# Performance work log

Measured on AMD Instinct MI355X. Metric: run time of the kernel, lower is better.

The kernel has to match this reference:

```python
import jax, jax.numpy as jnp
import numpy as np

N_NODES = 50000
N_EDGES = 800000
NODE_DIM = 128
EMBED_DIM = 128


def _gcn_conv(x, W, b, src, dst):
    """GCNConv: y = D^{-1/2} (A + I) D^{-1/2} X W + b (unit edge weights)."""
    n = x.shape[0]
    xw = x @ W  # [N, out]
    loop = jnp.arange(n, dtype=src.dtype)
    src2 = jnp.concatenate([src, loop])  # self-loops appended
    dst2 = jnp.concatenate([dst, loop])
    w2 = jnp.ones(src2.shape[0], dtype=xw.dtype)
    deg = jax.ops.segment_sum(w2, dst2, num_segments=n)
    dinv = jnp.where(deg > 0, jax.lax.rsqrt(deg), jnp.zeros_like(deg))
    norm = dinv[src2] * w2 * dinv[dst2]  # [E+N]
    out = jax.ops.segment_sum(norm[:, None] * xw[src2], dst2, num_segments=n)
    return out + b


def setup_inputs() -> dict:
    key = jax.random.key(0)
    ks = jax.random.split(key, 20)
    inp = {
        'node_feat': jax.random.normal(ks[0], (N_NODES, NODE_DIM), dtype=jnp.float32),
        'src': jax.random.randint(ks[1], (N_EDGES,), 0, N_NODES, dtype=jnp.int64) if jax.config.jax_enable_x64 else jax.random.randint(ks[1], (N_EDGES,), 0, N_NODES),
        'dst': jax.random.randint(ks[2], (N_EDGES,), 0, N_NODES),
        'h': jax.random.normal(ks[3], (N_NODES, EMBED_DIM), dtype=jnp.float32),
    }
    sc_in = 1.0 / np.sqrt(NODE_DIM)
    sc_2e = 1.0 / np.sqrt(2 * EMBED_DIM)
    sc_e = 1.0 / np.sqrt(EMBED_DIM)
    # conv weight/bias + gate linear weight/bias for z, r, h gates
    for i, g in enumerate(['z', 'r', 'hh']):
        inp[f'Wc_{g}'] = jax.random.normal(ks[4 + 4 * i], (NODE_DIM, EMBED_DIM), dtype=jnp.float32) * sc_in
        inp[f'bc_{g}'] = jnp.zeros((EMBED_DIM,), dtype=jnp.float32)
        inp[f'Wl_{g}'] = jax.random.normal(ks[5 + 4 * i], (2 * EMBED_DIM, EMBED_DIM), dtype=jnp.float32) * sc_2e
        inp[f'bl_{g}'] = jnp.zeros((EMBED_DIM,), dtype=jnp.float32)
    inp['W_lin'] = jax.random.normal(ks[16], (EMBED_DIM, EMBED_DIM), dtype=jnp.float32) * sc_e
    inp['b_lin'] = jnp.zeros((EMBED_DIM,), dtype=jnp.float32)
    return inp


def reference(node_feat, src, dst, h,
              Wc_z, bc_z, Wl_z, bl_z,
              Wc_r, bc_r, Wl_r, bl_r,
              Wc_hh, bc_hh, Wl_hh, bl_hh,
              W_lin, b_lin):
    # TGCN GRU cell
    cz = _gcn_conv(node_feat, Wc_z, bc_z, src, dst)
    Z = jax.nn.sigmoid(jnp.concatenate([cz, h], axis=1) @ Wl_z + bl_z)
    cr = _gcn_conv(node_feat, Wc_r, bc_r, src, dst)
    R = jax.nn.sigmoid(jnp.concatenate([cr, h], axis=1) @ Wl_r + bl_r)
    ch = _gcn_conv(node_feat, Wc_hh, bc_hh, src, dst)
    H_tilde = jnp.tanh(jnp.concatenate([ch, h * R], axis=1) @ Wl_hh + bl_hh)
    h_0 = Z * h + (1.0 - Z) * H_tilde
    # wrapper: relu + linear
    z_out = jax.nn.relu(h_0) @ W_lin + b_lin
    return (z_out, h_0)
```

## Files before the change

kernel.cpp:

```cpp
#include <hip/hip_runtime.h>
#include <math.h>

#define NN 50000
#define DD 128
#define EE 800000

typedef __attribute__((ext_vector_type(8))) short short8;
typedef __attribute__((ext_vector_type(4))) float f32x4;

__device__ __forceinline__ ushort f2bf(float f) {
    union { float f; unsigned u; } v; v.f = f;
    unsigned r = v.u + 0x7FFF + ((v.u >> 16) & 1);
    return (ushort)(r >> 16);
}

__global__ void k_cvt_deg(const float* __restrict__ X, ushort* __restrict__ Xb,
                          const int* __restrict__ dste, int* __restrict__ deg) {
    int i = blockIdx.x * 256 + threadIdx.x;
    float4 v = ((const float4*)X)[i];
    ushort4 u;
    u.x = f2bf(v.x); u.y = f2bf(v.y); u.z = f2bf(v.z); u.w = f2bf(v.w);
    ((ushort4*)Xb)[i] = u;
    if (i < EE) atomicAdd(&deg[dste[i]], 1);
}

__global__ void k_alloc(const int* __restrict__ deg, int* __restrict__ off,
                        int* __restrict__ cursor, float* __restrict__ dinv) {
    int n = blockIdx.x * 256 + threadIdx.x;
    int lane = threadIdx.x & 63;
    int d = (n < NN) ? deg[n] : 0;
    int x = d;
    #pragma unroll
    for (int o = 1; o < 64; o <<= 1) {
        int y = __shfl_up(x, o);
        if (lane >= o) x += y;
    }
    int total = __shfl(x, 63);
    int base = 0;
    if (lane == 0) base = atomicAdd(cursor, total);
    base = __shfl(base, 0);
    if (n < NN) {
        off[n] = base + x - d;
        dinv[n] = rsqrtf((float)d + 1.0f);
    }
}

__global__ void k_fill(const int* __restrict__ src, const int* __restrict__ dst,
                       const int* __restrict__ off, int* __restrict__ cur,
                       int* __restrict__ csr) {
    int e = blockIdx.x * 256 + threadIdx.x;
    if (e < EE) {
        int d = dst[e];
        int slot = atomicAdd(&cur[d], 1);
        csr[off[d] + slot] = src[e];
    }
}

__global__ __launch_bounds__(256) void k_gather(const ushort* __restrict__ Xb,
                                                const int* __restrict__ csr,
                                                const int* __restrict__ off,
                                                const int* __restrict__ deg,
                                                const float* __restrict__ dinv,
                                                ushort* __restrict__ AXb) {
    int tid = blockIdx.x * 256 + threadIdx.x;
    int n = tid >> 6, lane = tid & 63;
    if (n >= NN) return;
    float dd = dinv[n];
    uint a = *((const uint*)(Xb + (size_t)n * 128 + lane * 2));
    float acc0 = dd * dd * __uint_as_float(a << 16);
    float acc1 = dd * dd * __uint_as_float(a & 0xffff0000u);
    int o = off[n], cnt = deg[n];
    int i = 0;
    for (; i + 8 <= cnt; i += 8) {
        int s[8];
        #pragma unroll
        for (int u = 0; u < 8; u++) s[u] = csr[o + i + u];
        uint v[8];
        #pragma unroll
        for (int u = 0; u < 8; u++) v[u] = *((const uint*)(Xb + (size_t)s[u] * 128 + lane * 2));
        float c[8];
        #pragma unroll
        for (int u = 0; u < 8; u++) c[u] = dinv[s[u]] * dd;
        #pragma unroll
        for (int u = 0; u < 8; u++) {
            acc0 += c[u] * __uint_as_float(v[u] << 16);
            acc1 += c[u] * __uint_as_float(v[u] & 0xffff0000u);
        }
    }
    for (; i < cnt; i++) {
        int s = csr[o + i];
        float c = dinv[s] * dd;
        uint v = *((const uint*)(Xb + (size_t)s * 128 + lane * 2));
        acc0 += c * __uint_as_float(v << 16);
        acc1 += c * __uint_as_float(v & 0xffff0000u);
    }
    ushort2 u2; u2.x = f2bf(acc0); u2.y = f2bf(acc1);
    *((ushort2*)(AXb + (size_t)n * 128 + lane * 2)) = u2;
}

__global__ void k_prep(const float* __restrict__ Wc_z, const float* __restrict__ Wl_z,
                       const float* __restrict__ bc_z, const float* __restrict__ bl_z,
                       const float* __restrict__ Wc_r, const float* __restrict__ Wl_r,
                       const float* __restrict__ bc_r, const float* __restrict__ bl_r,
                       const float* __restrict__ Wc_h, const float* __restrict__ Wl_h,
                       const float* __restrict__ bc_h, const float* __restrict__ bl_h,
                       const float* __restrict__ W_lin,
                       ushort* __restrict__ WAs, ushort* __restrict__ WBs,
                       ushort* __restrict__ WLs, float* __restrict__ bA,
                       float* __restrict__ bB) {
    int idx = blockIdx.x * 256 + threadIdx.x;
    if (idx < 65536) {
        int k = idx >> 8, c = idx & 255, cc = c & 127;
        const float* Wc = (c < 128) ? Wc_z : Wc_r;
        const float* Wl = (c < 128) ? Wl_z : Wl_r;
        float v;
        if (k < 128) {
            float s = 0.f;
            for (int j = 0; j < 128; j++) s += Wc[k * 128 + j] * Wl[j * 128 + cc];
            v = s;
        } else {
            v = Wl[k * 128 + cc];
        }
        WAs[(k >> 5) * 8192 + (c >> 4) * 512 + (((k >> 3) & 3) * 16 + (c & 15)) * 8 + (k & 7)] = f2bf(v);
    } else if (idx < 98304) {
        int i2 = idx - 65536;
        int k = i2 >> 7, c = i2 & 127;
        float v;
        if (k < 128) {
            float s = 0.f;
            for (int j = 0; j < 128; j++) s += Wc_h[k * 128 + j] * Wl_h[j * 128 + c];
            v = s;
        } else {
            v = Wl_h[k * 128 + c];
        }
        WBs[(k >> 5) * 4096 + (c >> 4) * 512 + (((k >> 3) & 3) * 16 + (c & 15)) * 8 + (k & 7)] = f2bf(v);
    } else if (idx < 114688) {
        int i3 = idx - 98304;
        int k = i3 >> 7, c = i3 & 127;
        WLs[(k >> 5) * 4096 + (c >> 4) * 512 + (((k >> 3) & 3) * 16 + (c & 15)) * 8 + (k & 7)] = f2bf(W_lin[k * 128 + c]);
    } else if (idx < 114944) {
        int c = idx - 114688, cc = c & 127;
        const float* bc = (c < 128) ? bc_z : bc_r;
        const float* Wl = (c < 128) ? Wl_z : Wl_r;
        const float* bl = (c < 128) ? bl_z : bl_r;
        float s = bl[cc];
        for (int j = 0; j < 128; j++) s += bc[j] * Wl[j * 128 + cc];
        bA[c] = s;
    } else if (idx < 115072) {
        int c = idx - 114944;
        float s = bl_h[c];
        for (int j = 0; j < 128; j++) s += bc_h[j] * Wl_h[j * 128 + c];
        bB[c] = s;
    }
}

__global__ __launch_bounds__(256) void k_fused(const ushort* __restrict__ AXb,
                                               const float* __restrict__ h,
                                               const ushort* __restrict__ WAs,
                                               const ushort* __restrict__ WBs,
                                               const ushort* __restrict__ WLs,
                                               const float* __restrict__ bA,
                                               const float* __restrict__ bB,
                                               const float* __restrict__ b_lin,
                                               float* __restrict__ out_z,
                                               float* __restrict__ out_h) {
    __shared__ uint4 WbufV[2][1024];
    __shared__ __align__(16) ushort hRbuf[8192];

    const int tid = threadIdx.x;
    const int row0 = blockIdx.x * 64;
    const int lane = tid & 63, w = tid >> 6;
    const int tx = lane & 15, g = lane >> 4;
    const int arow = w * 16 + tx;
    const int gar = row0 + arow;
    const int drow = w * 16 + g * 4;
    const int aswz = (arow & 7) << 4;

    short8 z8 = {0, 0, 0, 0, 0, 0, 0, 0};
    short8 axf[4], hf[4];
    bool av = (gar < NN);
    #pragma unroll
    for (int ks = 0; ks < 4; ks++)
        axf[ks] = av ? *((const short8*)(AXb + (size_t)gar * 128 + ks * 32 + g * 8)) : z8;
    {
        const float4* hp = (const float4*)(h + (size_t)gar * 128);
        #pragma unroll
        for (int ks = 0; ks < 4; ks++) {
            if (av) {
                float4 u0 = hp[ks * 8 + g * 2];
                float4 u1 = hp[ks * 8 + g * 2 + 1];
                short8 t;
                t[0] = (short)f2bf(u0.x); t[1] = (short)f2bf(u0.y);
                t[2] = (short)f2bf(u0.z); t[3] = (short)f2bf(u0.w);
                t[4] = (short)f2bf(u1.x); t[5] = (short)f2bf(u1.y);
                t[6] = (short)f2bf(u1.z); t[7] = (short)f2bf(u1.w);
                hf[ks] = t;
            } else hf[ks] = z8;
        }
    }

    uint4 sr[4];
    const uint4* gwA = (const uint4*)WAs;

    #pragma unroll
    for (int j = 0; j < 4; j++) sr[j] = gwA[j * 256 + tid];
    #pragma unroll
    for (int j = 0; j < 4; j++) WbufV[0][j * 256 + tid] = sr[j];
    #pragma unroll
    for (int j = 0; j < 4; j++) sr[j] = gwA[1024 + j * 256 + tid];
    __syncthreads();

    f32x4 accA[16];
    #pragma unroll
    for (int ct = 0; ct < 16; ct++) accA[ct] = (f32x4){0.f, 0.f, 0.f, 0.f};

    #pragma unroll
    for (int ks = 0; ks < 8; ks++) {
        const int cur = ks & 1, nxt = cur ^ 1;
        if (ks < 7) {
            #pragma unroll
            for (int j = 0; j < 4; j++) WbufV[nxt][j * 256 + tid] = sr[j];
        }
        if (ks < 6) {
            #pragma unroll
            for (int j = 0; j < 4; j++) sr[j] = gwA[(ks + 2) * 1024 + j * 256 + tid];
        }
        const ushort* wbp = (const ushort*)WbufV[cur];
        short8 a = (ks < 4) ? axf[ks] : hf[ks - 4];
        #pragma unroll
        for (int ct = 0; ct < 16; ct++) {
            short8 b = *((const short8*)(wbp + ct * 512 + lane * 8));
            accA[ct] = __builtin_amdgcn_mfma_f32_16x16x32_bf16(a, b, accA[ct], 0, 0, 0);
        }
        __syncthreads();
    }

    float Zv[8][4], hv[8][4];
    #pragma unroll
    for (int ct = 0; ct < 8; ct++) {
        float bias = bA[ct * 16 + tx];
        #pragma unroll
        for (int r = 0; r < 4; r++)
            Zv[ct][r] = 1.f / (1.f + expf(-(accA[ct][r] + bias)));
    }
    #pragma unroll
    for (int ct = 0; ct < 8; ct++) {
        int cc = ct * 16 + tx;
        float bias = bA[128 + cc];
        #pragma unroll
        for (int r = 0; r < 4; r++) {
            int rr = drow + r, gr = row0 + rr;
            float hval = (gr < NN) ? h[(size_t)gr * 128 + cc] : 0.f;
            hv[ct][r] = hval;
            float R = 1.f / (1.f + expf(-(accA[8 + ct][r] + bias)));
            *((ushort*)((char*)hRbuf + rr * 256 + ((cc * 2) ^ ((rr & 7) << 4)))) = f2bf(hval * R);
        }
    }

    const uint4* gwB = (const uint4*)WBs;
    #pragma unroll
    for (int j = 0; j < 2; j++) sr[j] = gwB[j * 256 + tid];
    #pragma unroll
    for (int j = 0; j < 2; j++) WbufV[0][j * 256 + tid] = sr[j];
    #pragma unroll
    for (int j = 0; j < 2; j++) sr[j] = gwB[512 + j * 256 + tid];
    __syncthreads();

    f32x4 accB[8];
    #pragma unroll
    for (int ct = 0; ct < 8; ct++) accB[ct] = (f32x4){0.f, 0.f, 0.f, 0.f};

    #pragma unroll
    for (int ks = 0; ks < 8; ks++) {
        const int cur = ks & 1, nxt = cur ^ 1;
        if (ks < 7) {
            #pragma unroll
            for (int j = 0; j < 2; j++) WbufV[nxt][j * 256 + tid] = sr[j];
        }
        if (ks < 6) {
            #pragma unroll
            for (int j = 0; j < 2; j++) sr[j] = gwB[(ks + 2) * 512 + j * 256 + tid];
        }
        const ushort* wbp = (const ushort*)WbufV[cur];
        short8 a;
        if (ks < 4) {
            a = axf[ks];
        } else {
            int kk = ks - 4;
            a = *((const short8*)((const char*)hRbuf + arow * 256 + ((kk * 64 + g * 16) ^ aswz)));
        }
        #pragma unroll
        for (int ct = 0; ct < 8; ct++) {
            short8 b = *((const short8*)(wbp + ct * 512 + lane * 8));
            accB[ct] = __builtin_amdgcn_mfma_f32_16x16x32_bf16(a, b, accB[ct], 0, 0, 0);
        }
        __syncthreads();
    }

    #pragma unroll
    for (int ct = 0; ct < 8; ct++) {
        int cc = ct * 16 + tx;
        float bias = bB[cc];
        #pragma unroll
        for (int r = 0; r < 4; r++) {
            int rr = drow + r, gr = row0 + rr;
            float gv = accB[ct][r] + bias;
            float H = tanhf(gv);
            float Z = Zv[ct][r];
            float h0 = Z * hv[ct][r] + (1.f - Z) * H;
            if (gr < NN) out_h[(size_t)gr * 128 + cc] = h0;
            *((ushort*)((char*)hRbuf + rr * 256 + ((cc * 2) ^ ((rr & 7) << 4)))) = f2bf(fmaxf(h0, 0.f));
        }
    }

    const uint4* gwL = (const uint4*)WLs;
    #pragma unroll
    for (int j = 0; j < 2; j++) sr[j] = gwL[j * 256 + tid];
    #pragma unroll
    for (int j = 0; j < 2; j++) WbufV[0][j * 256 + tid] = sr[j];
    #pragma unroll
    for (int j = 0; j < 2; j++) sr[j] = gwL[512 + j * 256 + tid];
    __syncthreads();

    f32x4 accC[8];
    #pragma unroll
    for (int ct = 0; ct < 8; ct++) accC[ct] = (f32x4){0.f, 0.f, 0.f, 0.f};

    #pragma unroll
    for (int ks = 0; ks < 4; ks++) {
        const int cur = ks & 1, nxt = cur ^ 1;
        if (ks < 3) {
            #pragma unroll
            for (int j = 0; j < 2; j++) WbufV[nxt][j * 256 + tid] = sr[j];
        }
        if (ks < 2) {
            #pragma unroll
            for (int j = 0; j < 2; j++) sr[j] = gwL[(ks + 2) * 512 + j * 256 + tid];
        }
        const ushort* wbp = (const ushort*)WbufV[cur];
        short8 a = *((const short8*)((const char*)hRbuf + arow * 256 + ((ks * 64 + g * 16) ^ aswz)));
        #pragma unroll
        for (int ct = 0; ct < 8; ct++) {
            short8 b = *((const short8*)(wbp + ct * 512 + lane * 8));
            accC[ct] = __builtin_amdgcn_mfma_f32_16x16x32_bf16(a, b, accC[ct], 0, 0, 0);
        }
        __syncthreads();
    }

    #pragma unroll
    for (int ct = 0; ct < 8; ct++) {
        int cc = ct * 16 + tx;
        float bias = b_lin[cc];
        #pragma unroll
        for (int r = 0; r < 4; r++) {
            int gr = row0 + drow + r;
            if (gr < NN) out_z[(size_t)gr * 128 + cc] = accC[ct][r] + bias;
        }
    }
}


extern "C" void kernel_launch(void* const* d_in, const int* in_sizes, int n_in,
                              void* d_out, int out_size, void* d_ws, size_t ws_size,
                              hipStream_t stream) {
    const float* X    = (const float*)d_in[0];
    const int*   src  = (const int*)d_in[1];
    const int*   dst  = (const int*)d_in[2];
    const float* h    = (const float*)d_in[3];
    const float* Wc_z = (const float*)d_in[4];
    const float* bc_z = (const float*)d_in[5];
    const float* Wl_z = (const float*)d_in[6];
    const float* bl_z = (const float*)d_in[7];
    const float* Wc_r = (const float*)d_in[8];
    const float* bc_r = (const float*)d_in[9];
    const float* Wl_r = (const float*)d_in[10];
    const float* bl_r = (const float*)d_in[11];
    const float* Wc_h = (const float*)d_in[12];
    const float* bc_h = (const float*)d_in[13];
    const float* Wl_h = (const float*)d_in[14];
    const float* bl_h = (const float*)d_in[15];
    const float* W_lin = (const float*)d_in[16];
    const float* b_lin = (const float*)d_in[17];

    float* out_z = (float*)d_out;
    float* out_h = out_z + (size_t)NN * DD;

    float* ws = (float*)d_ws;
    float*  dinv   = ws;
    int*    deg    = (int*)(ws + 50048);
    int*    cur    = (int*)(ws + 100096);
    int*    cursor = (int*)(ws + 150144);
    int*    off    = (int*)(ws + 150208);
    int*    csr    = (int*)(ws + 200256);
    float*  bA     = ws + 1000320;
    float*  bB     = ws + 1000576;
    ushort* WAs    = (ushort*)(ws + 1000704);
    ushort* WBs    = (ushort*)(ws + 1033472);
    ushort* WLs    = (ushort*)(ws + 1049856);
    ushort* AXb    = (ushort*)(ws + 1058048);
    ushort* Xb     = (ushort*)(ws + 4258048);

    hipMemsetAsync(deg, 0, 100160 * sizeof(int), stream);
    k_prep<<<450, 256, 0, stream>>>(Wc_z, Wl_z, bc_z, bl_z, Wc_r, Wl_r, bc_r, bl_r,
                                    Wc_h, Wl_h, bc_h, bl_h, W_lin,
                                    WAs, WBs, WLs, bA, bB);
    k_cvt_deg<<<6250, 256, 0, stream>>>(X, Xb, dst, deg);
    k_alloc<<<196, 256, 0, stream>>>(deg, off, cursor, dinv);
    k_fill<<<3125, 256, 0, stream>>>(src, dst, off, cur, csr);
    k_gather<<<12500, 256, 0, stream>>>(Xb, csr, off, deg, dinv, AXb);
    k_fused<<<782, 256, 0, stream>>>(AXb, h, WAs, WBs, WLs, bA, bB, b_lin, out_z, out_h);
}
```

Baseline: 350.8 us.

## Merge prep into convert kernel, double fused-kernel row tile, scalarize gather offsets

The weight-prep kernel is folded into the X-conversion/degree kernel as extra blocks, removing one launch and letting the two run concurrently. The fused GRU kernel now handles 128 rows per block with two 16-row MFMA tiles per wave, so each staged weight fragment is reused twice. This halves the weight staging traffic per row at the cost of double the accumulator registers and shared memory, with launch bounds set for 2 blocks per CU. It also means 391 blocks instead of 782, which may underfill a 256-CU device. The gather kernel makes the per-node offset and degree wave-uniform through readfirstlane, and h is reloaded from memory in the final phase instead of being kept in registers.

Result: no change. 350.0 us (-0.2%).

```diff
diff --git a/kernel.cpp b/kernel.cpp
--- a/kernel.cpp
+++ b/kernel.cpp
@@ -14,101 +14,28 @@
     return (ushort)(r >> 16);
 }
 
-__global__ void k_cvt_deg(const float* __restrict__ X, ushort* __restrict__ Xb,
-                          const int* __restrict__ dste, int* __restrict__ deg) {
-    int i = blockIdx.x * 256 + threadIdx.x;
-    float4 v = ((const float4*)X)[i];
-    ushort4 u;
-    u.x = f2bf(v.x); u.y = f2bf(v.y); u.z = f2bf(v.z); u.w = f2bf(v.w);
-    ((ushort4*)Xb)[i] = u;
-    if (i < EE) atomicAdd(&deg[dste[i]], 1);
-}
-
-__global__ void k_alloc(const int* __restrict__ deg, int* __restrict__ off,
-                        int* __restrict__ cursor, float* __restrict__ dinv) {
-    int n = blockIdx.x * 256 + threadIdx.x;
-    int lane = threadIdx.x & 63;
-    int d = (n < NN) ? deg[n] : 0;
-    int x = d;
-    #pragma unroll
-    for (int o = 1; o < 64; o <<= 1) {
-        int y = __shfl_up(x, o);
-        if (lane >= o) x += y;
-    }
-    int total = __shfl(x, 63);
-    int base = 0;
-    if (lane == 0) base = atomicAdd(cursor, total);
-    base = __shfl(base, 0);
-    if (n < NN) {
-        off[n] = base + x - d;
-        dinv[n] = rsqrtf((float)d + 1.0f);
-    }
-}
-
-__global__ void k_fill(const int* __restrict__ src, const int* __restrict__ dst,
-                       const int* __restrict__ off, int* __restrict__ cur,
-                       int* __restrict__ csr) {
-    int e = blockIdx.x * 256 + threadIdx.x;
-    if (e < EE) {
-        int d = dst[e];
-        int slot = atomicAdd(&cur[d], 1);
-        csr[off[d] + slot] = src[e];
-    }
-}
-
-__global__ __launch_bounds__(256) void k_gather(const ushort* __restrict__ Xb,
-                                                const int* __restrict__ csr,
-                                                const int* __restrict__ off,
-                                                const int* __restrict__ deg,
-                                                const float* __restrict__ dinv,
-                                                ushort* __restrict__ AXb) {
-    int tid = blockIdx.x * 256 + threadIdx.x;
-    int n = tid >> 6, lane = tid & 63;
-    if (n >= NN) return;
-    float dd = dinv[n];
-    uint a = *((const uint*)(Xb + (size_t)n * 128 + lane * 2));
-    float acc0 = dd * dd * __uint_as_float(a << 16);
-    float acc1 = dd * dd * __uint_as_float(a & 0xffff0000u);
-    int o = off[n], cnt = deg[n];
-    int i = 0;
-    for (; i + 8 <= cnt; i += 8) {
-        int s[8];
-        #pragma unroll
-        for (int u = 0; u < 8; u++) s[u] = csr[o + i + u];
-        uint v[8];
-        #pragma unroll
-        for (int u = 0; u < 8; u++) v[u] = *((const uint*)(Xb + (size_t)s[u] * 128 + lane * 2));
-        float c[8];
-        #pragma unroll
-        for (int u = 0; u < 8; u++) c[u] = dinv[s[u]] * dd;
-        #pragma unroll
-        for (int u = 0; u < 8; u++) {
-            acc0 += c[u] * __uint_as_float(v[u] << 16);
-            acc1 += c[u] * __uint_as_float(v[u] & 0xffff0000u);
-        }
-    }
-    for (; i < cnt; i++) {
-        int s = csr[o + i];
-        float c = dinv[s] * dd;
-        uint v = *((const uint*)(Xb + (size_t)s * 128 + lane * 2));
-        acc0 += c * __uint_as_float(v << 16);
-        acc1 += c * __uint_as_float(v & 0xffff0000u);
-    }
-    ushort2 u2; u2.x = f2bf(acc0); u2.y = f2bf(acc1);
-    *((ushort2*)(AXb + (size_t)n * 128 + lane * 2)) = u2;
-}
-
-__global__ void k_prep(const float* __restrict__ Wc_z, const float* __restrict__ Wl_z,
-                       const float* __restrict__ bc_z, const float* __restrict__ bl_z,
-                       const float* __restrict__ Wc_r, const float* __restrict__ Wl_r,
-                       const float* __restrict__ bc_r, const float* __restrict__ bl_r,
-                       const float* __restrict__ Wc_h, const float* __restrict__ Wl_h,
-                       const float* __restrict__ bc_h, const float* __restrict__ bl_h,
-                       const float* __restrict__ W_lin,
-                       ushort* __restrict__ WAs, ushort* __restrict__ WBs,
-                       ushort* __restrict__ WLs, float* __restrict__ bA,
-                       float* __restrict__ bB) {
-    int idx = blockIdx.x * 256 + threadIdx.x;
+__global__ void k_cvtprep(const float* __restrict__ X, ushort* __restrict__ Xb,
+                          const int* __restrict__ dste, int* __restrict__ deg,
+                          const float* __restrict__ Wc_z, const float* __restrict__ Wl_z,
+                          const float* __restrict__ bc_z, const float* __restrict__ bl_z,
+                          const float* __restrict__ Wc_r, const float* __restrict__ Wl_r,
+                          const float* __restrict__ bc_r, const float* __restrict__ bl_r,
+                          const float* __restrict__ Wc_h, const float* __restrict__ Wl_h,
+                          const float* __restrict__ bc_h, const float* __restrict__ bl_h,
+                          const float* __restrict__ W_lin,
+                          ushort* __restrict__ WAs, ushort* __restrict__ WBs,
+                          ushort* __restrict__ WLs, float* __restrict__ bA,
+                          float* __restrict__ bB) {
+    if (blockIdx.x < 6250) {
+        int i = blockIdx.x * 256 + threadIdx.x;
+        float4 v = ((const float4*)X)[i];
+        ushort4 u;
+        u.x = f2bf(v.x); u.y = f2bf(v.y); u.z = f2bf(v.z); u.w = f2bf(v.w);
+        ((ushort4*)Xb)[i] = u;
+        if (i < EE) atomicAdd(&deg[dste[i]], 1);
+        return;
+    }
+    int idx = (blockIdx.x - 6250) * 256 + threadIdx.x;
     if (idx < 65536) {
         int k = idx >> 8, c = idx & 255, cc = c & 127;
         const float* Wc = (c < 128) ? Wc_z : Wc_r;
@@ -154,48 +81,130 @@
     }
 }
 
-__global__ __launch_bounds__(256) void k_fused(const ushort* __restrict__ AXb,
-                                               const float* __restrict__ h,
-                                               const ushort* __restrict__ WAs,
-                                               const ushort* __restrict__ WBs,
-                                               const ushort* __restrict__ WLs,
-                                               const float* __restrict__ bA,
-                                               const float* __restrict__ bB,
-                                               const float* __restrict__ b_lin,
-                                               float* __restrict__ out_z,
-                                               float* __restrict__ out_h) {
+__global__ void k_alloc(const int* __restrict__ deg, int* __restrict__ off,
+                        int* __restrict__ cursor, float* __restrict__ dinv) {
+    int n = blockIdx.x * 256 + threadIdx.x;
+    int lane = threadIdx.x & 63;
+    int d = (n < NN) ? deg[n] : 0;
+    int x = d;
+    #pragma unroll
+    for (int o = 1; o < 64; o <<= 1) {
+        int y = __shfl_up(x, o);
+        if (lane >= o) x += y;
+    }
+    int total = __shfl(x, 63);
+    int base = 0;
+    if (lane == 0) base = atomicAdd(cursor, total);
+    base = __shfl(base, 0);
+    if (n < NN) {
+        off[n] = base + x - d;
+        dinv[n] = rsqrtf((float)d + 1.0f);
+    }
+}
+
+__global__ void k_fill(const int* __restrict__ src, const int* __restrict__ dst,
+                       const int* __restrict__ off, int* __restrict__ cur,
+                       int* __restrict__ csr) {
+    int e = blockIdx.x * 256 + threadIdx.x;
+    if (e < EE) {
+        int d = dst[e];
+        int slot = atomicAdd(&cur[d], 1);
+        csr[off[d] + slot] = src[e];
+    }
+}
+
+__global__ __launch_bounds__(256) void k_gather(const ushort* __restrict__ Xb,
+                                                const int* __restrict__ csr,
+                                                const int* __restrict__ off,
+                                                const int* __restrict__ deg,
+                                                const float* __restrict__ dinv,
+                                                ushort* __restrict__ AXb) {
+    int tid = blockIdx.x * 256 + threadIdx.x;
+    int n = tid >> 6, lane = tid & 63;
+    if (n >= NN) return;
+    int o   = __builtin_amdgcn_readfirstlane(off[n]);
+    int cnt = __builtin_amdgcn_readfirstlane(deg[n]);
+    float dd = dinv[n];
+    uint a = *((const uint*)(Xb + (size_t)n * 128 + lane * 2));
+    float acc0 = dd * dd * __uint_as_float(a << 16);
+    float acc1 = dd * dd * __uint_as_float(a & 0xffff0000u);
+    int i = 0;
+    for (; i + 8 <= cnt; i += 8) {
+        int s[8];
+        #pragma unroll
+        for (int u = 0; u < 8; u++) s[u] = csr[o + i + u];
+        uint v[8];
+        #pragma unroll
+        for (int u = 0; u < 8; u++) v[u] = *((const uint*)(Xb + (size_t)s[u] * 128 + lane * 2));
+        float c[8];
+        #pragma unroll
+        for (int u = 0; u < 8; u++) c[u] = dinv[s[u]] * dd;
+        #pragma unroll
+        for (int u = 0; u < 8; u++) {
+            acc0 += c[u] * __uint_as_float(v[u] << 16);
+            acc1 += c[u] * __uint_as_float(v[u] & 0xffff0000u);
+        }
+    }
+    for (; i < cnt; i++) {
+        int s = csr[o + i];
+        float c = dinv[s] * dd;
+        uint v = *((const uint*)(Xb + (size_t)s * 128 + lane * 2));
+        acc0 += c * __uint_as_float(v << 16);
+        acc1 += c * __uint_as_float(v & 0xffff0000u);
+    }
+    ushort2 u2; u2.x = f2bf(acc0); u2.y = f2bf(acc1);
+    *((ushort2*)(AXb + (size_t)n * 128 + lane * 2)) = u2;
+}
+
+__global__ __launch_bounds__(256, 2) void k_fused(const ushort* __restrict__ AXb,
+                                                  const float* __restrict__ h,
+                                                  const ushort* __restrict__ WAs,
+                                                  const ushort* __restrict__ WBs,
+                                                  const ushort* __restrict__ WLs,
+                                                  const float* __restrict__ bA,
+                                                  const float* __restrict__ bB,
+                                                  const float* __restrict__ b_lin,
+                                                  float* __restrict__ out_z,
+                                                  float* __restrict__ out_h) {
     __shared__ uint4 WbufV[2][1024];
-    __shared__ __align__(16) ushort hRbuf[8192];
+    __shared__ __align__(16) ushort hRbuf[16384];
 
     const int tid = threadIdx.x;
-    const int row0 = blockIdx.x * 64;
+    const int row0 = blockIdx.x * 128;
     const int lane = tid & 63, w = tid >> 6;
     const int tx = lane & 15, g = lane >> 4;
-    const int arow = w * 16 + tx;
-    const int gar = row0 + arow;
-    const int drow = w * 16 + g * 4;
-    const int aswz = (arow & 7) << 4;
+
+    int arow[2], gar[2], aswz[2];
+    bool av[2];
+    #pragma unroll
+    for (int t = 0; t < 2; t++) {
+        arow[t] = w * 32 + t * 16 + tx;
+        gar[t]  = row0 + arow[t];
+        av[t]   = gar[t] < NN;
+        aswz[t] = (arow[t] & 7) << 4;
+    }
+    const int drow0 = w * 32 + g * 4;
 
     short8 z8 = {0, 0, 0, 0, 0, 0, 0, 0};
-    short8 axf[4], hf[4];
-    bool av = (gar < NN);
-    #pragma unroll
-    for (int ks = 0; ks < 4; ks++)
-        axf[ks] = av ? *((const short8*)(AXb + (size_t)gar * 128 + ks * 32 + g * 8)) : z8;
-    {
-        const float4* hp = (const float4*)(h + (size_t)gar * 128);
+    short8 axf[2][4], hf[2][4];
+    #pragma unroll
+    for (int t = 0; t < 2; t++) {
+        #pragma unroll
+        for (int ks = 0; ks < 4; ks++)
+            axf[t][ks] = av[t] ? *((const short8*)(AXb + (size_t)gar[t] * 128 + ks * 32 + g * 8)) : z8;
+        const float4* hp = (const float4*)(h + (size_t)gar[t] * 128);
         #pragma unroll
         for (int ks = 0; ks < 4; ks++) {
-            if (av) {
+            if (av[t]) {
                 float4 u0 = hp[ks * 8 + g * 2];
                 float4 u1 = hp[ks * 8 + g * 2 + 1];
-                short8 t;
-                t[0] = (short)f2bf(u0.x); t[1] = (short)f2bf(u0.y);
-                t[2] = (short)f2bf(u0.z); t[3] = (short)f2bf(u0.w);
-                t[4] = (short)f2bf(u1.x); t[5] = (short)f2bf(u1.y);
-                t[6] = (short)f2bf(u1.z); t[7] = (short)f2bf(u1.w);
-                hf[ks] = t;
-            } else hf[ks] = z8;
+                short8 tt;
+                tt[0] = (short)f2bf(u0.x); tt[1] = (short)f2bf(u0.y);
+                tt[2] = (short)f2bf(u0.z); tt[3] = (short)f2bf(u0.w);
+                tt[4] = (short)f2bf(u1.x); tt[5] = (short)f2bf(u1.y);
+                tt[6] = (short)f2bf(u1.z); tt[7] = (short)f2bf(u1.w);
+                hf[t][ks] = tt;
+            } else hf[t][ks] = z8;
         }
     }
 
@@ -210,9 +219,11 @@
     for (int j = 0; j < 4; j++) sr[j] = gwA[1024 + j * 256 + tid];
     __syncthreads();
 
-    f32x4 accA[16];
-    #pragma unroll
-    for (int ct = 0; ct < 16; ct++) accA[ct] = (f32x4){0.f, 0.f, 0.f, 0.f};
+    f32x4 accA[2][16];
+    #pragma unroll
+    for (int t = 0; t < 2; t++)
+        #pragma unroll
+        for (int ct = 0; ct < 16; ct++) accA[t][ct] = (f32x4){0.f, 0.f, 0.f, 0.f};
 
     #pragma unroll
     for (int ks = 0; ks < 8; ks++) {
@@ -226,36 +237,41 @@
             for (int j = 0; j < 4; j++) sr[j] = gwA[(ks + 2) * 1024 + j * 256 + tid];
         }
         const ushort* wbp = (const ushort*)WbufV[cur];
-        short8 a = (ks < 4) ? axf[ks] : hf[ks - 4];
+        short8 a0 = (ks < 4) ? axf[0][ks] : hf[0][ks - 4];
+        short8 a1 = (ks < 4) ? axf[1][ks] : hf[1][ks - 4];
         #pragma unroll
         for (int ct = 0; ct < 16; ct++) {
             short8 b = *((const short8*)(wbp + ct * 512 + lane * 8));
-            accA[ct] = __builtin_amdgcn_mfma_f32_16x16x32_bf16(a, b, accA[ct], 0, 0, 0);
+            accA[0][ct] = __builtin_amdgcn_mfma_f32_16x16x32_bf16(a0, b, accA[0][ct], 0, 0, 0);
+            accA[1][ct] = __builtin_amdgcn_mfma_f32_16x16x32_bf16(a1, b, accA[1][ct], 0, 0, 0);
         }
         __syncthreads();
     }
 
-    float Zv[8][4], hv[8][4];
-    #pragma unroll
-    for (int ct = 0; ct < 8; ct++) {
-        float bias = bA[ct * 16 + tx];
-        #pragma unroll
-        for (int r = 0; r < 4; r++)
-            Zv[ct][r] = 1.f / (1.f + expf(-(accA[ct][r] + bias)));
-    }
-    #pragma unroll
-    for (int ct = 0; ct < 8; ct++) {
-        int cc = ct * 16 + tx;
-        float bias = bA[128 + cc];
-        #pragma unroll
-        for (int r = 0; r < 4; r++) {
-            int rr = drow + r, gr = row0 + rr;
-            float hval = (gr < NN) ? h[(size_t)gr * 128 + cc] : 0.f;
-            hv[ct][r] = hval;
-            float R = 1.f / (1.f + expf(-(accA[8 + ct][r] + bias)));
-            *((ushort*)((char*)hRbuf + rr * 256 + ((cc * 2) ^ ((rr & 7) << 4)))) = f2bf(hval * R);
-        }
-    }
+    float Zv[2][8][4];
+    #pragma unroll
+    for (int t = 0; t < 2; t++)
+        #pragma unroll
+        for (int ct = 0; ct < 8; ct++) {
+            float bias = bA[ct * 16 + tx];
+            #pragma unroll
+            for (int r = 0; r < 4; r++)
+                Zv[t][ct][r] = 1.f / (1.f + expf(-(accA[t][ct][r] + bias)));
+        }
+    #pragma unroll
+    for (int t = 0; t < 2; t++)
+        #pragma unroll
+        for (int ct = 0; ct < 8; ct++) {
+            int cc = ct * 16 + tx;
+            float bias = bA[128 + cc];
+            #pragma unroll
+            for (int r = 0; r < 4; r++) {
+                int rr = drow0 + t * 16 + r, gr = row0 + rr;
+                float hval = (gr < NN) ? h[(size_t)gr * 128 + cc] : 0.f;
+                float R = 1.f / (1.f + expf(-(accA[t][8 + ct][r] + bias)));
+                *((ushort*)((char*)hRbuf + rr * 256 + ((cc * 2) ^ ((rr & 7) << 4)))) = f2bf(hval * R);
+            }
+        }
 
     const uint4* gwB = (const uint4*)WBs;
     #pragma unroll
@@ -266,9 +282,11 @@
     for (int j = 0; j < 2; j++) sr[j] = gwB[512 + j * 256 + tid];
     __syncthreads();
 
-    f32x4 accB[8];
-    #pragma unroll
-    for (int ct = 0; ct < 8; ct++) accB[ct] = (f32x4){0.f, 0.f, 0.f, 0.f};
+    f32x4 accB[2][8];
+    #pragma unroll
+    for (int t = 0; t < 2; t++)
+        #pragma unroll
+        for (int ct = 0; ct < 8; ct++) accB[t][ct] = (f32x4){0.f, 0.f, 0.f, 0.f};
 
     #pragma unroll
     for (int ks = 0; ks < 8; ks++) {
@@ -282,36 +300,41 @@
             for (int j = 0; j < 2; j++) sr[j] = gwB[(ks + 2) * 512 + j * 256 + tid];
         }
         const ushort* wbp = (const ushort*)WbufV[cur];
-        short8 a;
+        short8 a0, a1;
         if (ks < 4) {
-            a = axf[ks];
+            a0 = axf[0][ks]; a1 = axf[1][ks];
         } else {
             int kk = ks - 4;
-            a = *((const short8*)((const char*)hRbuf + arow * 256 + ((kk * 64 + g * 16) ^ aswz)));
+            a0 = *((const short8*)((const char*)hRbuf + arow[0] * 256 + ((kk * 64 + g * 16) ^ aswz[0])));
+            a1 = *((const short8*)((const char*)hRbuf + arow[1] * 256 + ((kk * 64 + g * 16) ^ aswz[1])));
         }
         #pragma unroll
         for (int ct = 0; ct < 8; ct++) {
             short8 b = *((const short8*)(wbp + ct * 512 + lane * 8));
-            accB[ct] = __builtin_amdgcn_mfma_f32_16x16x32_bf16(a, b, accB[ct], 0, 0, 0);
+            accB[0][ct] = __builtin_amdgcn_mfma_f32_16x16x32_bf16(a0, b, accB[0][ct], 0, 0, 0);
+            accB[1][ct] = __builtin_amdgcn_mfma_f32_16x16x32_bf16(a1, b, accB[1][ct], 0, 0, 0);
         }
         __syncthreads();
     }
 
     #pragma unroll
-    for (int ct = 0; ct < 8; ct++) {
-        int cc = ct * 16 + tx;
-        float bias = bB[cc];
-        #pragma unroll
-        for (int r = 0; r < 4; r++) {
-            int rr = drow + r, gr = row0 + rr;
-            float gv = accB[ct][r] + bias;
-            float H = tanhf(gv);
-            float Z = Zv[ct][r];
-            float h0 = Z * hv[ct][r] + (1.f - Z) * H;
-            if (gr < NN) out_h[(size_t)gr * 128 + cc] = h0;
-            *((ushort*)((char*)hRbuf + rr * 256 + ((cc * 2) ^ ((rr & 7) << 4)))) = f2bf(fmaxf(h0, 0.f));
-        }
-    }
+    for (int t = 0; t < 2; t++)
+        #pragma unroll
+        for (int ct = 0; ct < 8; ct++) {
+            int cc = ct * 16 + tx;
+            float bias = bB[cc];
+            #pragma unroll
+            for (int r = 0; r < 4; r++) {
+                int rr = drow0 + t * 16 + r, gr = row0 + rr;
+                float hval = (gr < NN) ? h[(size_t)gr * 128 + cc] : 0.f;
+                float gv = accB[t][ct][r] + bias;
+                float H = tanhf(gv);
+                float Z = Zv[t][ct][r];
+                float h0 = Z * hval + (1.f - Z) * H;
+                if (gr < NN) out_h[(size_t)gr * 128 + cc] = h0;
+                *((ushort*)((char*)hRbuf + rr * 256 + ((cc * 2) ^ ((rr & 7) << 4)))) = f2bf(fmaxf(h0, 0.f));
+            }
+        }
 
     const uint4* gwL = (const uint4*)WLs;
     #pragma unroll
@@ -322,9 +345,11 @@
     for (int j = 0; j < 2; j++) sr[j] = gwL[512 + j * 256 + tid];
     __syncthreads();
 
-    f32x4 accC[8];
-    #pragma unroll
-    for (int ct = 0; ct < 8; ct++) accC[ct] = (f32x4){0.f, 0.f, 0.f, 0.f};
+    f32x4 accC[2][8];
+    #pragma unroll
+    for (int t = 0; t < 2; t++)
+        #pragma unroll
+        for (int ct = 0; ct < 8; ct++) accC[t][ct] = (f32x4){0.f, 0.f, 0.f, 0.f};
 
     #pragma unroll
     for (int ks = 0; ks < 4; ks++) {
@@ -338,25 +363,29 @@
             for (int j = 0; j < 2; j++) sr[j] = gwL[(ks + 2) * 512 + j * 256 + tid];
         }
         const ushort* wbp = (const ushort*)WbufV[cur];
-        short8 a = *((const short8*)((const char*)hRbuf + arow * 256 + ((ks * 64 + g * 16) ^ aswz)));
+        short8 a0 = *((const short8*)((const char*)hRbuf + arow[0] * 256 + ((ks * 64 + g * 16) ^ aswz[0])));
+        short8 a1 = *((const short8*)((const char*)hRbuf + arow[1] * 256 + ((ks * 64 + g * 16) ^ aswz[1])));
         #pragma unroll
         for (int ct = 0; ct < 8; ct++) {
             short8 b = *((const short8*)(wbp + ct * 512 + lane * 8));
-            accC[ct] = __builtin_amdgcn_mfma_f32_16x16x32_bf16(a, b, accC[ct], 0, 0, 0);
+            accC[0][ct] = __builtin_amdgcn_mfma_f32_16x16x32_bf16(a0, b, accC[0][ct], 0, 0, 0);
+            accC[1][ct] = __builtin_amdgcn_mfma_f32_16x16x32_bf16(a1, b, accC[1][ct], 0, 0, 0);
         }
         __syncthreads();
     }
 
     #pragma unroll
-    for (int ct = 0; ct < 8; ct++) {
-        int cc = ct * 16 + tx;
-        float bias = b_lin[cc];
-        #pragma unroll
-        for (int r = 0; r < 4; r++) {
-            int gr = row0 + drow + r;
-            if (gr < NN) out_z[(size_t)gr * 128 + cc] = accC[ct][r] + bias;
-        }
-    }
+    for (int t = 0; t < 2; t++)
+        #pragma unroll
+        for (int ct = 0; ct < 8; ct++) {
+            int cc = ct * 16 + tx;
+            float bias = b_lin[cc];
+            #pragma unroll
+            for (int r = 0; r < 4; r++) {
+                int gr = row0 + drow0 + t * 16 + r;
+                if (gr < NN) out_z[(size_t)gr * 128 + cc] = accC[t][ct][r] + bias;
+            }
+        }
 }
 
 
@@ -401,12 +430,12 @@
     ushort* Xb     = (ushort*)(ws + 4258048);
 
     hipMemsetAsync(deg, 0, 100160 * sizeof(int), stream);
-    k_prep<<<450, 256, 0, stream>>>(Wc_z, Wl_z, bc_z, bl_z, Wc_r, Wl_r, bc_r, bl_r,
-                                    Wc_h, Wl_h, bc_h, bl_h, W_lin,
-                                    WAs, WBs, WLs, bA, bB);
-    k_cvt_deg<<<6250, 256, 0, stream>>>(X, Xb, dst, deg);
+    k_cvtprep<<<6700, 256, 0, stream>>>(X, Xb, dst, deg,
+                                        Wc_z, Wl_z, bc_z, bl_z, Wc_r, Wl_r, bc_r, bl_r,
+                                        Wc_h, Wl_h, bc_h, bl_h, W_lin,
+                                        WAs, WBs, WLs, bA, bB);
     k_alloc<<<196, 256, 0, stream>>>(deg, off, cursor, dinv);
     k_fill<<<3125, 256, 0, stream>>>(src, dst, off, cur, csr);
     k_gather<<<12500, 256, 0, stream>>>(Xb, csr, off, deg, dinv, AXb);
-    k_fused<<<782, 256, 0, stream>>>(AXb, h, WAs, WBs, WLs, bA, bB, b_lin, out_z, out_h);
-}
+    k_fused<<<391, 256, 0, stream>>>(AXb, h, WAs, WBs, WLs, bA, bB, b_lin, out_z, out_h);
+}
```
